# Kernel tuning notes

Hardware: AMD Instinct MI355X
Metric: run time of the kernel (lower is better)

The kernel has to match this reference:

```python
import jax, jax.numpy as jnp
import numpy as np

C, L, M, DEPTH = 32, 4, 128, 7
DIM = (L ** (DEPTH + 1) - 1) // (L - 1)  # 21845 nodes, complete 4-ary tree, BFS order


def _level_starts(dim, fanout):
    # start offset of each BFS level of a complete `fanout`-ary tree
    starts = [0]
    n = 1
    while starts[-1] + n < dim:
        starts.append(starts[-1] + n)
        n *= fanout
    starts.append(dim)
    return starts  # level d occupies [starts[d], starts[d+1])


def setup_inputs() -> dict:
    key = jax.random.key(0)
    ks = jax.random.split(key, 5)
    return {
        "labels": jax.random.randint(ks[0], (DIM,), 0, M, dtype=jnp.int32),
        "A": jax.random.normal(ks[1], (C, C, L), jnp.float32),
        "B": jax.random.normal(ks[2], (C, M), jnp.float32),
        "Pi": jax.random.normal(ks[3], (C, L), jnp.float32),
        "SP": jax.random.normal(ks[4], (L,), jnp.float32),
    }


def _htmm_log_likelihood(labels, A, B, Pi, SP):
    dim = labels.shape[0]
    c, m = B.shape
    fan = A.shape[2]
    starts = _level_starts(dim, fan)
    D = len(starts) - 2  # deepest level index (leaves)

    # softmax reparameterization (dims as in torch source)
    smA = jax.nn.softmax(A, axis=0)   # (C,C,L)
    smB = jax.nn.softmax(B, axis=1)   # (C,M)
    smPi = jax.nn.softmax(Pi, axis=0)  # (C,L)
    smSP = jax.nn.softmax(SP, axis=0)  # (L,)

    n_leaves = starts[D + 1] - starts[D]
    leaf_pos = jnp.arange(n_leaves) % fan          # child position of each leaf
    leaf_labels = labels[starts[D]:]

    # ---- upward pass ----
    beta_leaf = smPi[:, leaf_pos].T * smB[:, leaf_labels].T  # (n_leaves,C)
    beta_leaf = beta_leaf / beta_leaf.sum(1, keepdims=True)
    beta = jnp.zeros((dim, c), A.dtype).at[starts[D]:].set(beta_leaf)
    t_beta = jnp.zeros((dim, c), A.dtype)
    A_SP = smA * smSP[None, None, :]  # (C,C,L): SP[pos] * A[:,:,pos]

    for d in range(D - 1, -1, -1):
        n_p = starts[d + 1] - starts[d]
        beta_ch = beta[starts[d + 1]:starts[d + 2]].reshape(n_p, fan, c)  # (P,L,C)
        # t_beta_u[i] = sum_l SP[l] * sum_j A[i,j,l] * beta_child_l[j]
        tb = jnp.einsum('ijl,plj->pi', A_SP, beta_ch)  # (P,C)
        bl = tb * smB[:, labels[starts[d]:starts[d + 1]]].T
        bl = bl / bl.sum(1, keepdims=True)
        t_beta = t_beta.at[starts[d]:starts[d + 1]].set(tb)
        beta = beta.at[starts[d]:starts[d + 1]].set(bl)

    # ---- downward pass ----
    eps = jnp.zeros((dim, c), A.dtype).at[0].set(beta[0])
    t_eps = jnp.zeros((dim, c, c, fan), A.dtype)
    for d in range(D):
        n_p = starts[d + 1] - starts[d]
        beta_ch = beta[starts[d + 1]:starts[d + 2]].reshape(n_p, fan, c)  # (P,L,C)
        eps_pa = eps[starts[d]:starts[d + 1]]    # (P,C)
        tb_pa = t_beta[starts[d]:starts[d + 1]]  # (P,C)
        # t_eps_u[j,i,l] = beta[ch_l,i] * SP[l]*A[j,i,l] * eps_u[j] / t_beta_u[j]
        te = (beta_ch.transpose(0, 2, 1)[:, None, :, :]   # (P,1,C_i,L)
              * A_SP[None]                                  # (1,C_j,C_i,L)
              * (eps_pa / tb_pa)[:, :, None, None])         # (P,C_j,1,1)
        t_eps = t_eps.at[starts[d]:starts[d + 1]].set(te)
        eps_ch = te.sum(1).transpose(0, 2, 1).reshape(-1, c)  # sum_j -> (P,L,C) -> (P*L,C)
        eps = eps.at[starts[d + 1]:starts[d + 2]].set(eps_ch)

    # ---- log-likelihood ----
    ll = (t_eps * jnp.log(smA)[None]).sum()
    ll = ll + (eps * jnp.log(smB)[:, labels].T).sum()
    ll = ll + (eps[starts[D]:] * jnp.log(smPi)[:, leaf_pos].T).sum()
    ll = ll + (t_eps * jnp.log(smSP)[None, None, None, :]).sum()
    return ll


def reference(labels, A, B, Pi, SP):
    return _htmm_log_likelihood(labels, A, B, Pi, SP)
```

## Files before the change

kernel.cpp:

```cpp
#include <hip/hip_runtime.h>


static constexpr int OFF_B4   = 0;
static constexpr int OFF_PART = 8192;
static constexpr int IC2      = 9760;
static constexpr int IROOT2   = 10272;

__device__ __forceinline__ float rsum32(float v) {
#pragma unroll
  for (int k = 1; k <= 16; k <<= 1) v += __shfl_xor(v, k);
  return v;
}
__device__ __forceinline__ void rsum32x2(float& a, float& b) {
#pragma unroll
  for (int k = 1; k <= 16; k <<= 1) { a += __shfl_xor(a, k); b += __shfl_xor(b, k); }
}
__device__ __forceinline__ void rsum32x4(float& a, float& b, float& c, float& d) {
#pragma unroll
  for (int k = 1; k <= 16; k <<= 1) {
    a += __shfl_xor(a, k); b += __shfl_xor(b, k);
    c += __shfl_xor(c, k); d += __shfl_xor(d, k);
  }
}
__device__ __forceinline__ float4 exp4f(float4 v) {
  return make_float4(__expf(v.x), __expf(v.y), __expf(v.z), __expf(v.w));
}

#define W_DECL float4 Wr0, Wr1, Wr2, Wr3, Wr4, Wr5, Wr6, Wr7, Wr8, Wr9,     \
    Wr10, Wr11, Wr12, Wr13, Wr14, Wr15, Wr16, Wr17, Wr18, Wr19, Wr20, Wr21, \
    Wr22, Wr23, Wr24, Wr25, Wr26, Wr27, Wr28, Wr29, Wr30, Wr31;

#define REPW(X) X(0,Wr0) X(1,Wr1) X(2,Wr2) X(3,Wr3) X(4,Wr4) X(5,Wr5)       \
    X(6,Wr6) X(7,Wr7) X(8,Wr8) X(9,Wr9) X(10,Wr10) X(11,Wr11) X(12,Wr12)    \
    X(13,Wr13) X(14,Wr14) X(15,Wr15) X(16,Wr16) X(17,Wr17) X(18,Wr18)       \
    X(19,Wr19) X(20,Wr20) X(21,Wr21) X(22,Wr22) X(23,Wr23) X(24,Wr24)       \
    X(25,Wr25) X(26,Wr26) X(27,Wr27) X(28,Wr28) X(29,Wr29) X(30,Wr30)       \
    X(31,Wr31)

#define REPQ(X) X(0,Wr0,Wr1,Wr2,Wr3) X(1,Wr4,Wr5,Wr6,Wr7)                   \
    X(2,Wr8,Wr9,Wr10,Wr11) X(3,Wr12,Wr13,Wr14,Wr15) X(4,Wr16,Wr17,Wr18,Wr19)\
    X(5,Wr20,Wr21,Wr22,Wr23) X(6,Wr24,Wr25,Wr26,Wr27) X(7,Wr28,Wr29,Wr30,Wr31)

#define WLD_B(J, WJ) WJ = *(const float4*)(scrW_ + 4 * (J));
#define W_LOADUP { const float* scrW_ = scr + lane * 132; REPW(WLD_B) }

#define DOT_B(J, WJ) { const float4 x_ = *(const float4*)(dXp_ + 4 * (J));   \
    dt0_ = fmaf(WJ.x, x_.x, dt0_); dt1_ = fmaf(WJ.y, x_.y, dt1_);            \
    dt2_ = fmaf(WJ.z, x_.z, dt2_); dt3_ = fmaf(WJ.w, x_.w, dt3_); }
#define DOT128M(OUT, XP) { const float* dXp_ = (XP);                         \
    float dt0_ = 0.f, dt1_ = 0.f, dt2_ = 0.f, dt3_ = 0.f;                    \
    REPW(DOT_B) (OUT) = (dt0_ + dt1_) + (dt2_ + dt3_); }

#define DOTX2_B(J, WJ) {                                                     \
    const float4 x_ = *(const float4*)(dXp0_ + 4 * (J));                     \
    const float4 y_ = *(const float4*)(dXp1_ + 4 * (J));                     \
    da0_ = fmaf(WJ.x, x_.x, da0_); db0_ = fmaf(WJ.x, y_.x, db0_);            \
    da1_ = fmaf(WJ.y, x_.y, da1_); db1_ = fmaf(WJ.y, y_.y, db1_);            \
    da2_ = fmaf(WJ.z, x_.z, da2_); db2_ = fmaf(WJ.z, y_.z, db2_);            \
    da3_ = fmaf(WJ.w, x_.w, da3_); db3_ = fmaf(WJ.w, y_.w, db3_); }
#define DOT128X2M(O0, O1, XP0, XP1) {                                        \
    const float* dXp0_ = (XP0); const float* dXp1_ = (XP1);                  \
    float da0_ = 0.f, da1_ = 0.f, da2_ = 0.f, da3_ = 0.f;                    \
    float db0_ = 0.f, db1_ = 0.f, db2_ = 0.f, db3_ = 0.f;                    \
    REPW(DOTX2_B) (O0) = (da0_ + da1_) + (da2_ + da3_);                      \
    (O1) = (db0_ + db1_) + (db2_ + db3_); }

#define WO_B(Q, WA, WB, WC, WD) {                                            \
    const float4 rv_ = *(const float4*)(rbp_ + 4 * (Q));                     \
    ww0_ = fmaf(WA.x, rv_.x, ww0_); ww1_ = fmaf(WA.y, rv_.x, ww1_);          \
    ww2_ = fmaf(WA.z, rv_.x, ww2_); ww3_ = fmaf(WA.w, rv_.x, ww3_);          \
    ww0_ = fmaf(WB.x, rv_.y, ww0_); ww1_ = fmaf(WB.y, rv_.y, ww1_);          \
    ww2_ = fmaf(WB.z, rv_.y, ww2_); ww3_ = fmaf(WB.w, rv_.y, ww3_);          \
    ww0_ = fmaf(WC.x, rv_.z, ww0_); ww1_ = fmaf(WC.y, rv_.z, ww1_);          \
    ww2_ = fmaf(WC.z, rv_.z, ww2_); ww3_ = fmaf(WC.w, rv_.z, ww3_);          \
    ww0_ = fmaf(WD.x, rv_.w, ww0_); ww1_ = fmaf(WD.y, rv_.w, ww1_);          \
    ww2_ = fmaf(WD.z, rv_.w, ww2_); ww3_ = fmaf(WD.w, rv_.w, ww3_); }
#define WONLY128M(W, RBP) { const float* rbp_ = (RBP);                       \
    float ww0_ = 0.f, ww1_ = 0.f, ww2_ = 0.f, ww3_ = 0.f;                    \
    REPQ(WO_B) (W)[0] = ww0_; (W)[1] = ww1_; (W)[2] = ww2_; (W)[3] = ww3_; }

#define WU_SUB(ROW, WX, RC) {                                                \
    const float4 av_ = *(const float4*)(ALGp_ + (ROW) * 128);                \
    ww0_ = fmaf(WX.x, RC, ww0_); uu0_ = fmaf(av_.x, RC, uu0_);               \
    ww1_ = fmaf(WX.y, RC, ww1_); uu1_ = fmaf(av_.y, RC, uu1_);               \
    ww2_ = fmaf(WX.z, RC, ww2_); uu2_ = fmaf(av_.z, RC, uu2_);               \
    ww3_ = fmaf(WX.w, RC, ww3_); uu3_ = fmaf(av_.w, RC, uu3_); }
#define WU_B(Q, WA, WB, WC, WD) {                                            \
    const float4 rv_ = *(const float4*)(rbp_ + 4 * (Q));                     \
    WU_SUB(4 * (Q) + 0, WA, rv_.x) WU_SUB(4 * (Q) + 1, WB, rv_.y)            \
    WU_SUB(4 * (Q) + 2, WC, rv_.z) WU_SUB(4 * (Q) + 3, WD, rv_.w) }
#define WU128M(W, U, RBP) { const float* rbp_ = (RBP);                       \
    const float* ALGp_ = scr + lane * 4;                                     \
    float ww0_ = 0.f, ww1_ = 0.f, ww2_ = 0.f, ww3_ = 0.f;                    \
    float uu0_ = 0.f, uu1_ = 0.f, uu2_ = 0.f, uu3_ = 0.f;                    \
    REPQ(WU_B) (W)[0] = ww0_; (W)[1] = ww1_; (W)[2] = ww2_; (W)[3] = ww3_;   \
    (U)[0] = uu0_; (U)[1] = uu1_; (U)[2] = uu2_; (U)[3] = uu3_; }

#define WUX2_SUB(ROW, WX, RC0, RC1) {                                        \
    const float4 av_ = *(const float4*)(ALGp_ + (ROW) * 128);                \
    wa0_ = fmaf(WX.x, RC0, wa0_); wb0_ = fmaf(WX.x, RC1, wb0_);              \
    ua0_ = fmaf(av_.x, RC0, ua0_); ub0_ = fmaf(av_.x, RC1, ub0_);            \
    wa1_ = fmaf(WX.y, RC0, wa1_); wb1_ = fmaf(WX.y, RC1, wb1_);              \
    ua1_ = fmaf(av_.y, RC0, ua1_); ub1_ = fmaf(av_.y, RC1, ub1_);            \
    wa2_ = fmaf(WX.z, RC0, wa2_); wb2_ = fmaf(WX.z, RC1, wb2_);              \
    ua2_ = fmaf(av_.z, RC0, ua2_); ub2_ = fmaf(av_.z, RC1, ub2_);            \
    wa3_ = fmaf(WX.w, RC0, wa3_); wb3_ = fmaf(WX.w, RC1, wb3_);              \
    ua3_ = fmaf(av_.w, RC0, ua3_); ub3_ = fmaf(av_.w, RC1, ub3_); }
#define WUX2_B(Q, WA, WB, WC, WD) {                                          \
    const float4 rv0_ = *(const float4*)(rbp0_ + 4 * (Q));                   \
    const float4 rv1_ = *(const float4*)(rbp1_ + 4 * (Q));                   \
    WUX2_SUB(4 * (Q) + 0, WA, rv0_.x, rv1_.x)                                \
    WUX2_SUB(4 * (Q) + 1, WB, rv0_.y, rv1_.y)                                \
    WUX2_SUB(4 * (Q) + 2, WC, rv0_.z, rv1_.z)                                \
    WUX2_SUB(4 * (Q) + 3, WD, rv0_.w, rv1_.w) }
#define WU128X2M(W0, U0, W1, U1, RBP0, RBP1) {                               \
    const float* rbp0_ = (RBP0); const float* rbp1_ = (RBP1);                \
    const float* ALGp_ = scr + lane * 4;                                     \
    float wa0_ = 0.f, wa1_ = 0.f, wa2_ = 0.f, wa3_ = 0.f;                    \
    float ua0_ = 0.f, ua1_ = 0.f, ua2_ = 0.f, ua3_ = 0.f;                    \
    float wb0_ = 0.f, wb1_ = 0.f, wb2_ = 0.f, wb3_ = 0.f;                    \
    float ub0_ = 0.f, ub1_ = 0.f, ub2_ = 0.f, ub3_ = 0.f;                    \
    REPQ(WUX2_B)                                                             \
    (W0)[0] = wa0_; (W0)[1] = wa1_; (W0)[2] = wa2_; (W0)[3] = wa3_;          \
    (U0)[0] = ua0_; (U0)[1] = ua1_; (U0)[2] = ua2_; (U0)[3] = ua3_;          \
    (W1)[0] = wb0_; (W1)[1] = wb1_; (W1)[2] = wb2_; (W1)[3] = wb3_;          \
    (U1)[0] = ub0_; (U1)[1] = ub1_; (U1)[2] = ub2_; (U1)[3] = ub3_; }

#define WRD_B(J, WJ) { const float4 av = A4[(J) * 32 + lane];                \
    const float4 e = exp4f(av);                                              \
    const float4 asp = make_float4(e.x * inv4.x, e.y * inv4.y,               \
                                   e.z * inv4.z, e.w * inv4.w);              \
    WJ = asp;                                                                \
    if (grp == ((J) >> 1))                                                   \
      *(float4*)(scr + (J) * 128 + lane * 4) =                               \
          make_float4(asp.x * (av.x - sub4.x), asp.y * (av.y - sub4.y),      \
                      asp.z * (av.z - sub4.z), asp.w * (av.w - sub4.w)); }

__global__ __launch_bounds__(256, 1) void k_up(const int* __restrict__ labels,
                                               const float* __restrict__ A,
                                               const float* __restrict__ B,
                                               const float* __restrict__ Pi,
                                               const float* __restrict__ SP,
                                               float* __restrict__ ws) {
  __shared__ __align__(16) float scr[4224];
  __shared__ __align__(16) float regB[4224];
  __shared__ __align__(16) float sPt[132];
  __shared__ int labs[425];
  const int t = threadIdx.x, lane = t & 31, grp = t >> 5;
  const int s = blockIdx.x;
  int* wsi = (int*)ws;
  const float4* A4 = (const float4*)A;
  const float4* B4 = (const float4*)B;

  if (t < 16) wsi[IC2 + 32 * t] = 0;
  else if (t == 16) wsi[IROOT2] = 0;

  const float sv0 = SP[0], sv1 = SP[1], sv2 = SP[2], sv3 = SP[3];
  const float sp0 = __expf(sv0), sp1 = __expf(sv1), sp2 = __expf(sv2), sp3 = __expf(sv3);
  const float spsum = sp0 + sp1 + sp2 + sp3;
  const float spinv = 1.f / spsum;
  float4 c4 = make_float4(0.f, 0.f, 0.f, 0.f);
  for (int i = 0; i < 32; ++i) {
    const float4 e = exp4f(A4[i * 32 + lane]);
    c4.x += e.x; c4.y += e.y; c4.z += e.z; c4.w += e.w;
  }
  const float4 inv4 = make_float4(sp0 * spinv / c4.x, sp1 * spinv / c4.y,
                                  sp2 * spinv / c4.z, sp3 * spinv / c4.w);
#pragma unroll
  for (int k = 0; k < 4; ++k) {
    const int i = grp * 4 + k;
    const float4 e = exp4f(A4[i * 32 + lane]);
    *(float4*)(scr + i * 132 + 4 * lane) =
        make_float4(e.x * inv4.x, e.y * inv4.y, e.z * inv4.z, e.w * inv4.w);
  }
#pragma unroll
  for (int rI = 0; rI < 4; ++rI) {
    const int i = grp + rI * 8;
    const float4 e = exp4f(B4[i * 32 + lane]);
    const float sinv = 1.f / rsum32(e.x + e.y + e.z + e.w);
    regB[(4 * lane + 0) * 33 + i] = e.x * sinv;
    regB[(4 * lane + 1) * 33 + i] = e.y * sinv;
    regB[(4 * lane + 2) * 33 + i] = e.z * sinv;
    regB[(4 * lane + 3) * 33 + i] = e.w * sinv;
  }
  if (grp < 4) {
    const float e = __expf(Pi[lane * 4 + grp]);
    sPt[grp * 33 + lane] = e / rsum32(e);
  }
  if (t < 84) {
    int g, d;
    if (t < 4) { g = 341 + 4 * s + t; d = 341 + t; }
    else if (t < 20) { g = 1365 + 16 * s + (t - 4); d = 345 + (t - 4); }
    else { g = 5461 + 64 * s + (t - 20); d = 361 + (t - 20); }
    labs[d] = labels[g];
  }
  if (t == 84) labs[85 + (s & 255)] = labels[85 + s];
  __syncthreads();
  W_DECL
  W_LOADUP
  __syncthreads();

#pragma unroll
  for (int h = 0; h < 2; ++h) {
    const int q0 = grp + 32 * h, q1 = q0 + 8, q2 = q0 + 16, q3 = q0 + 24;
    float v0 = sPt[(q0 & 3) * 33 + lane] * regB[labs[361 + q0] * 33 + lane];
    float v1 = sPt[(q1 & 3) * 33 + lane] * regB[labs[361 + q1] * 33 + lane];
    float v2 = sPt[(q2 & 3) * 33 + lane] * regB[labs[361 + q2] * 33 + lane];
    float v3 = sPt[(q3 & 3) * 33 + lane] * regB[labs[361 + q3] * 33 + lane];
    float s0 = v0, s1 = v1, s2 = v2, s3 = v3;
    rsum32x4(s0, s1, s2, s3);
    scr[(q0 >> 2) * 128 + lane * 4 + (q0 & 3)] = v0 / s0;
    scr[(q1 >> 2) * 128 + lane * 4 + (q1 & 3)] = v1 / s1;
    scr[(q2 >> 2) * 128 + lane * 4 + (q2 & 3)] = v2 / s2;
    scr[(q3 >> 2) * 128 + lane * 4 + (q3 & 3)] = v3 / s3;
  }
  __syncthreads();
  {
    const int p0 = grp, p1 = grp + 8;
    float tb0, tb1;
    DOT128X2M(tb0, tb1, scr + p0 * 128, scr + p1 * 128)
    float bl0 = tb0 * regB[labs[345 + p0] * 33 + lane];
    float bl1 = tb1 * regB[labs[345 + p1] * 33 + lane];
    float s0 = bl0, s1 = bl1;
    rsum32x2(s0, s1);
    bl0 /= s0; bl1 /= s1;
    scr[2048 + (p0 >> 2) * 128 + lane * 4 + (p0 & 3)] = bl0;
    scr[2048 + (p1 >> 2) * 128 + lane * 4 + (p1 & 3)] = bl1;
  }
  __syncthreads();
  if (grp < 4) {
    float tb;
    DOT128M(tb, scr + 2048 + grp * 128)
    float bl = tb * regB[labs[341 + grp] * 33 + lane];
    bl /= rsum32(bl);
    scr[2560 + lane * 4 + grp] = bl;
  }
  __syncthreads();
  if (grp == 0) {
    float tb;
    DOT128M(tb, scr + 2560)
    float bl = tb * regB[labs[85 + (s & 255)] * 33 + lane];
    bl /= rsum32(bl);
    ws[OFF_B4 + s * 32 + lane] = bl;
  }
}

__global__ __launch_bounds__(512, 1)
void k_down(const int* __restrict__ labels,
            const float* __restrict__ A,
            const float* __restrict__ B,
            const float* __restrict__ Pi,
            const float* __restrict__ SP,
            float* __restrict__ ws,
            float* __restrict__ out) {
  __shared__ __align__(16) float scr[6144];
  __shared__ __align__(16) float regB[4224];
  __shared__ __align__(16) float sPt[132];
  __shared__ __align__(16) float tbrT[2720];
  __shared__ __align__(16) float tbS[672];
  __shared__ __align__(16) float ownb[32];
  __shared__ __align__(16) float r_buf[512];
  __shared__ int labs[425];
  __shared__ int fin;
  const int t = threadIdx.x, lane = t & 31, grp = t >> 5;
  const int s = blockIdx.x;
  int* wsi = (int*)ws;
  double* partd = (double*)(ws + OFF_PART);
  const float4* A4 = (const float4*)A;
  const float4* B4 = (const float4*)B;

  float pf0[8], pf1[8];
#pragma unroll
  for (int h = 0; h < 2; ++h) {
    const int p0 = grp + 32 * h, p1 = p0 + 16;
#pragma unroll
    for (int l = 0; l < 4; ++l) {
      pf0[h * 4 + l] = ws[OFF_B4 + (p0 * 4 + l) * 32 + lane];
      pf1[h * 4 + l] = ws[OFF_B4 + (p1 * 4 + l) * 32 + lane];
    }
  }

  const float sv0 = SP[0], sv1 = SP[1], sv2 = SP[2], sv3 = SP[3];
  const float sp0 = __expf(sv0), sp1 = __expf(sv1), sp2 = __expf(sv2), sp3 = __expf(sv3);
  const float spsum = sp0 + sp1 + sp2 + sp3;
  const float spinv = 1.f / spsum;
  const float lss = __logf(spsum);
  float4 c4 = make_float4(0.f, 0.f, 0.f, 0.f);
  for (int i = 0; i < 32; ++i) {
    const float4 e = exp4f(A4[i * 32 + lane]);
    c4.x += e.x; c4.y += e.y; c4.z += e.z; c4.w += e.w;
  }
  const float4 inv4 = make_float4(sp0 * spinv / c4.x, sp1 * spinv / c4.y,
                                  sp2 * spinv / c4.z, sp3 * spinv / c4.w);
  const float4 sub4 = make_float4(__logf(c4.x) - (sv0 - lss), __logf(c4.y) - (sv1 - lss),
                                  __logf(c4.z) - (sv2 - lss), __logf(c4.w) - (sv3 - lss));
#pragma unroll
  for (int k = 0; k < 2; ++k) {
    const int i = grp * 2 + k;
    const float4 e = exp4f(A4[i * 32 + lane]);
    *(float4*)(scr + i * 132 + 4 * lane) =
        make_float4(e.x * inv4.x, e.y * inv4.y, e.z * inv4.z, e.w * inv4.w);
  }
#pragma unroll
  for (int rI = 0; rI < 2; ++rI) {
    const int i = grp + rI * 16;
    const float4 e = exp4f(B4[i * 32 + lane]);
    const float sinv = 1.f / rsum32(e.x + e.y + e.z + e.w);
    regB[(4 * lane + 0) * 33 + i] = e.x * sinv;
    regB[(4 * lane + 1) * 33 + i] = e.y * sinv;
    regB[(4 * lane + 2) * 33 + i] = e.z * sinv;
    regB[(4 * lane + 3) * 33 + i] = e.w * sinv;
  }
  if (grp < 4) {
    const float e = __expf(Pi[lane * 4 + grp]);
    sPt[grp * 33 + lane] = e / rsum32(e);
  }
  for (int idx = t; idx < 341; idx += 512) labs[idx] = labels[idx];
  if (t < 84) {
    int g, d;
    if (t < 4) { g = 341 + 4 * s + t; d = 341 + t; }
    else if (t < 20) { g = 1365 + 16 * s + (t - 4); d = 345 + (t - 4); }
    else { g = 5461 + 64 * s + (t - 20); d = 361 + (t - 20); }
    labs[d] = labels[g];
  }
  __syncthreads();
  W_DECL
  W_LOADUP
  __syncthreads();

  {
    const int q0 = grp, q1 = grp + 16, q2 = grp + 32, q3 = grp + 48;
    float v0 = sPt[(q0 & 3) * 33 + lane] * regB[labs[361 + q0] * 33 + lane];
    float v1 = sPt[(q1 & 3) * 33 + lane] * regB[labs[361 + q1] * 33 + lane];
    float v2 = sPt[(q2 & 3) * 33 + lane] * regB[labs[361 + q2] * 33 + lane];
    float v3 = sPt[(q3 & 3) * 33 + lane] * regB[labs[361 + q3] * 33 + lane];
    float s0 = v0, s1 = v1, s2 = v2, s3 = v3;
    rsum32x4(s0, s1, s2, s3);
    scr[(q0 >> 2) * 128 + lane * 4 + (q0 & 3)] = v0 / s0;
    scr[(q1 >> 2) * 128 + lane * 4 + (q1 & 3)] = v1 / s1;
    scr[(q2 >> 2) * 128 + lane * 4 + (q2 & 3)] = v2 / s2;
    scr[(q3 >> 2) * 128 + lane * 4 + (q3 & 3)] = v3 / s3;
  }
  __syncthreads();
  if (grp < 8) {
    const int p0 = grp, p1 = grp + 8;
    float tb0, tb1;
    DOT128X2M(tb0, tb1, scr + p0 * 128, scr + p1 * 128)
    float bl0 = tb0 * regB[labs[345 + p0] * 33 + lane];
    float bl1 = tb1 * regB[labs[345 + p1] * 33 + lane];
    float s0 = bl0, s1 = bl1;
    rsum32x2(s0, s1);
    bl0 /= s0; bl1 /= s1;
    tbS[(5 + p0) * 32 + lane] = tb0;
    tbS[(5 + p1) * 32 + lane] = tb1;
    scr[2048 + (p0 >> 2) * 128 + lane * 4 + (p0 & 3)] = bl0;
    scr[2048 + (p1 >> 2) * 128 + lane * 4 + (p1 & 3)] = bl1;
  }
  __syncthreads();
  if (grp < 4) {
    float tb;
    DOT128M(tb, scr + 2048 + grp * 128)
    float bl = tb * regB[labs[341 + grp] * 33 + lane];
    bl /= rsum32(bl);
    tbS[(1 + grp) * 32 + lane] = tb;
    scr[2560 + lane * 4 + grp] = bl;
  }
  __syncthreads();
  if (grp == 0) {
    float tb;
    DOT128M(tb, scr + 2560)
    float bl = tb * regB[labs[85 + s] * 33 + lane];
    bl /= rsum32(bl);
    tbS[lane] = tb;
    ownb[lane] = bl;
  }
  __syncthreads();

#pragma unroll
  for (int h = 0; h < 2; ++h) {
    const int p0 = grp + 32 * h, p1 = p0 + 16;
    float* st0 = scr + grp * 128;
    float* st1 = scr + 2048 + grp * 128;
#pragma unroll
    for (int l = 0; l < 4; ++l) {
      st0[lane * 4 + l] = pf0[h * 4 + l];
      st1[lane * 4 + l] = pf1[h * 4 + l];
    }
    float tb0, tb1;
    DOT128X2M(tb0, tb1, st0, st1)
    float bl0 = tb0 * regB[labs[21 + p0] * 33 + lane];
    float bl1 = tb1 * regB[labs[21 + p1] * 33 + lane];
    float s0 = bl0, s1 = bl1;
    rsum32x2(s0, s1);
    bl0 /= s0; bl1 /= s1;
    tbrT[(21 + p0) * 32 + lane] = tb0;
    tbrT[(21 + p1) * 32 + lane] = tb1;
    scr[4096 + (p0 >> 2) * 128 + lane * 4 + (p0 & 3)] = bl0;
    scr[4096 + (p1 >> 2) * 128 + lane * 4 + (p1 & 3)] = bl1;
  }
  __syncthreads();
  {
    const int p = grp;
    float tb;
    DOT128M(tb, scr + 4096 + p * 128)
    float bl = tb * regB[labs[5 + p] * 33 + lane];
    bl /= rsum32(bl);
    tbrT[(5 + p) * 32 + lane] = tb;
    scr[(p >> 2) * 128 + lane * 4 + (p & 3)] = bl;
  }
  __syncthreads();
  if (grp < 4) {
    float tb;
    DOT128M(tb, scr + grp * 128)
    float bl = tb * regB[labs[1 + grp] * 33 + lane];
    bl /= rsum32(bl);
    tbrT[(1 + grp) * 32 + lane] = tb;
    scr[512 + lane * 4 + grp] = bl;
  }
  __syncthreads();
  if (grp == 0) { float tb; DOT128M(tb, scr + 512) tbrT[lane] = tb; }
  __syncthreads();

  for (int idx = t; idx < 4224; idx += 512) regB[idx] = __logf(regB[idx]);
  if (t < 132) sPt[t] = __logf(sPt[t]);
  REPW(WRD_B)
  __syncthreads();

  double ll = 0.0;
  float eps4own = 0.f;
  if (grp < 4) {
    const int n1 = 1 + (s >> 6), n2 = 5 + (s >> 4), n3 = 21 + (s >> 2);
    const int a0 = s >> 6, a1 = (s >> 4) & 3, a2 = (s >> 2) & 3, a3 = s & 3;
    float w[4], uv[4];
    float* rb = r_buf + grp * 32;

    float tbv = tbrT[lane];
    float bcv = tbv * __expf(regB[labs[0] * 33 + lane]);
    bcv /= rsum32(bcv);
    rb[lane] = bcv / tbv;
    if (grp == 0 && s == 0) {
      ll += (double)(bcv * regB[labs[0] * 33 + lane]);
      WU128M(w, uv, rb)
      const float lb0 = regB[labs[1] * 33 + lane], lb1 = regB[labs[2] * 33 + lane];
      const float lb2 = regB[labs[3] * 33 + lane], lb3 = regB[labs[4] * 33 + lane];
      float b0 = tbrT[1 * 32 + lane] * __expf(lb0);
      float b1 = tbrT[2 * 32 + lane] * __expf(lb1);
      float b2 = tbrT[3 * 32 + lane] * __expf(lb2);
      float b3 = tbrT[4 * 32 + lane] * __expf(lb3);
      float s0 = b0, s1 = b1, s2 = b2, s3 = b3;
      rsum32x4(s0, s1, s2, s3);
      b0 /= s0; b1 /= s1; b2 /= s2; b3 /= s3;
      ll += (double)(b0 * uv[0]) + (double)(b0 * w[0] * lb0);
      ll += (double)(b1 * uv[1]) + (double)(b1 * w[1] * lb1);
      ll += (double)(b2 * uv[2]) + (double)(b2 * w[2] * lb2);
      ll += (double)(b3 * uv[3]) + (double)(b3 * w[3] * lb3);
    } else {
      WONLY128M(w, rb)
    }

    tbv = tbrT[n1 * 32 + lane];
    bcv = tbv * __expf(regB[labs[n1] * 33 + lane]);
    bcv /= rsum32(bcv);
    rb[lane] = (bcv * w[a0]) / tbv;
    if (grp == 1 && (s & 63) == 0) {
      WU128M(w, uv, rb)
      const int cb = 5 + 4 * (s >> 6);
      const float lb0 = regB[labs[cb + 0] * 33 + lane], lb1 = regB[labs[cb + 1] * 33 + lane];
      const float lb2 = regB[labs[cb + 2] * 33 + lane], lb3 = regB[labs[cb + 3] * 33 + lane];
      float b0 = tbrT[(cb + 0) * 32 + lane] * __expf(lb0);
      float b1 = tbrT[(cb + 1) * 32 + lane] * __expf(lb1);
      float b2 = tbrT[(cb + 2) * 32 + lane] * __expf(lb2);
      float b3 = tbrT[(cb + 3) * 32 + lane] * __expf(lb3);
      float s0 = b0, s1 = b1, s2 = b2, s3 = b3;
      rsum32x4(s0, s1, s2, s3);
      b0 /= s0; b1 /= s1; b2 /= s2; b3 /= s3;
      ll += (double)(b0 * uv[0]) + (double)(b0 * w[0] * lb0);
      ll += (double)(b1 * uv[1]) + (double)(b1 * w[1] * lb1);
      ll += (double)(b2 * uv[2]) + (double)(b2 * w[2] * lb2);
      ll += (double)(b3 * uv[3]) + (double)(b3 * w[3] * lb3);
    } else {
      WONLY128M(w, rb)
    }

    tbv = tbrT[n2 * 32 + lane];
    bcv = tbv * __expf(regB[labs[n2] * 33 + lane]);
    bcv /= rsum32(bcv);
    rb[lane] = (bcv * w[a1]) / tbv;
    if (grp == 2 && (s & 15) == 0) {
      WU128M(w, uv, rb)
      const int cb = 21 + 4 * (s >> 4);
      const float lb0 = regB[labs[cb + 0] * 33 + lane], lb1 = regB[labs[cb + 1] * 33 + lane];
      const float lb2 = regB[labs[cb + 2] * 33 + lane], lb3 = regB[labs[cb + 3] * 33 + lane];
      float b0 = tbrT[(cb + 0) * 32 + lane] * __expf(lb0);
      float b1 = tbrT[(cb + 1) * 32 + lane] * __expf(lb1);
      float b2 = tbrT[(cb + 2) * 32 + lane] * __expf(lb2);
      float b3 = tbrT[(cb + 3) * 32 + lane] * __expf(lb3);
      float s0 = b0, s1 = b1, s2 = b2, s3 = b3;
      rsum32x4(s0, s1, s2, s3);
      b0 /= s0; b1 /= s1; b2 /= s2; b3 /= s3;
      ll += (double)(b0 * uv[0]) + (double)(b0 * w[0] * lb0);
      ll += (double)(b1 * uv[1]) + (double)(b1 * w[1] * lb1);
      ll += (double)(b2 * uv[2]) + (double)(b2 * w[2] * lb2);
      ll += (double)(b3 * uv[3]) + (double)(b3 * w[3] * lb3);
    } else {
      WONLY128M(w, rb)
    }

    tbv = tbrT[n3 * 32 + lane];
    bcv = tbv * __expf(regB[labs[n3] * 33 + lane]);
    bcv /= rsum32(bcv);
    rb[lane] = (bcv * w[a2]) / tbv;
    if (grp == 3 && (s & 3) == 0) {
      WU128M(w, uv, rb)
      const int cb = s & ~3;
#pragma unroll
      for (int l = 0; l < 4; ++l) {
        const int ci = cb + l;
        const float bc = ws[OFF_B4 + ci * 32 + lane];
        const float e = bc * w[l];
        ll += (double)(bc * uv[l]) + (double)(e * regB[labs[85 + ci] * 33 + lane]);
      }
    } else {
      WONLY128M(w, rb)
    }
    eps4own = ownb[lane] * w[a3];
  }
  __syncthreads();

  if (grp == 0) {
    r_buf[lane] = eps4own / tbS[lane];
    float w[4], u[4];
    WU128M(w, u, r_buf)
#pragma unroll
    for (int l = 0; l < 4; ++l) {
      const int lab = labs[341 + l];
      const float tbv = tbS[(1 + l) * 32 + lane];
      float bcv = tbv * __expf(regB[lab * 33 + lane]);
      bcv /= rsum32(bcv);
      const float e = bcv * w[l];
      ll += (double)(bcv * u[l]) + (double)(e * regB[lab * 33 + lane]);
      tbS[(1 + l) * 32 + lane] = e / tbv;
    }
  }
  __syncthreads();
  if (grp < 4) {
    const int p = grp;
    r_buf[p * 32 + lane] = tbS[(1 + p) * 32 + lane];
    float w[4], u[4];
    WU128M(w, u, r_buf + p * 32)
#pragma unroll
    for (int l = 0; l < 4; ++l) {
      const int q = p * 4 + l;
      const int lab = labs[345 + q];
      const float tbv = tbS[(5 + q) * 32 + lane];
      float bcv = tbv * __expf(regB[lab * 33 + lane]);
      bcv /= rsum32(bcv);
      const float e = bcv * w[l];
      ll += (double)(bcv * u[l]) + (double)(e * regB[lab * 33 + lane]);
      tbS[(5 + q) * 32 + lane] = e / tbv;
    }
  }
  __syncthreads();
  if (grp < 8) {
    const int p0 = grp, p1 = grp + 8;
    float* rb0 = r_buf + grp * 32;
    float* rb1 = r_buf + 256 + grp * 32;
    rb0[lane] = tbS[(5 + p0) * 32 + lane];
    rb1[lane] = tbS[(5 + p1) * 32 + lane];
    float w0[4], u0[4], w1[4], u1[4];
    WU128X2M(w0, u0, w1, u1, rb0, rb1)
#pragma unroll
    for (int l = 0; l < 4; ++l) {
      const int q0 = p0 * 4 + l, q1 = p1 * 4 + l;
      const float lb0 = regB[labs[361 + q0] * 33 + lane];
      const float lb1 = regB[labs[361 + q1] * 33 + lane];
      const float lp = sPt[l * 33 + lane];
      float b0 = __expf(lp + lb0);
      float b1 = __expf(lp + lb1);
      float s0 = b0, s1 = b1;
      rsum32x2(s0, s1);
      b0 /= s0; b1 /= s1;
      const float e0 = b0 * w0[l], e1 = b1 * w1[l];
      ll += (double)(b0 * u0[l]) + (double)(e0 * lb0) + (double)(e0 * lp);
      ll += (double)(b1 * u1[l]) + (double)(e1 * lb1) + (double)(e1 * lp);
    }
  }

#pragma unroll
  for (int k = 32; k >= 1; k >>= 1) ll += __shfl_xor(ll, k);
  double* rbd = (double*)r_buf;
  __syncthreads();
  if ((t & 63) == 0) rbd[t >> 6] = ll;
  __syncthreads();
  if (t == 0) {
    partd[s] = ((rbd[0] + rbd[1]) + (rbd[2] + rbd[3])) +
               ((rbd[4] + rbd[5]) + (rbd[6] + rbd[7]));
    __threadfence();
    int f = 0;
    if (atomicAdd(&wsi[IC2 + 32 * (s >> 4)], 1) == 15)
      if (atomicAdd(&wsi[IROOT2], 1) == 15) f = 1;
    fin = f;
  }
  __syncthreads();
  if (fin) {
    __threadfence();
    if (t < 64) {
      double v = 0.0;
      for (int k = t; k < 256; k += 64) v += partd[k];
#pragma unroll
      for (int k = 32; k >= 1; k >>= 1) v += __shfl_xor(v, k);
      if (t == 0) out[0] = (float)v;
    }
  }
}

extern "C" void kernel_launch(void* const* d_in, const int* in_sizes, int n_in,
                              void* d_out, int out_size, void* d_ws, size_t ws_size,
                              hipStream_t stream) {
  (void)in_sizes; (void)n_in; (void)out_size; (void)ws_size;
  const int* labels = (const int*)d_in[0];
  const float* A = (const float*)d_in[1];
  const float* B = (const float*)d_in[2];
  const float* Pi = (const float*)d_in[3];
  const float* SP = (const float*)d_in[4];
  float* ws = (float*)d_ws;
  float* out = (float*)d_out;

  hipLaunchKernelGGL(k_up, dim3(256), dim3(256), 0, stream,
                     labels, A, B, Pi, SP, ws);
  hipLaunchKernelGGL(k_down, dim3(256), dim3(512), 0, stream,
                     labels, A, B, Pi, SP, ws, out);
}
```

Baseline: 106.4 us.

## Precompute softmax tables and subtree t_beta in up pass, reuse in down pass

The up kernel now runs with 512 threads. Block 0 writes the normalized A_SP, the softmaxed B, log B, log Pi and the A*logA tables to workspace. Every block also stores its subtree's t_beta values. The down kernel loads these instead of recomputing the softmaxes and the bottom upward levels, which removes redundant exp/log work and one set of dot products per block. In exchange it adds workspace traffic and depends on a workspace-size check; when the workspace is too small it falls back to the old kernels.

```diff
diff --git a/kernel.cpp b/kernel.cpp
--- a/kernel.cpp
+++ b/kernel.cpp
@@ -5,6 +5,13 @@
 static constexpr int OFF_PART = 8192;
 static constexpr int IC2      = 9760;
 static constexpr int IROOT2   = 10272;
+static constexpr int OFF_ASP  = 10304;
+static constexpr int OFF_RB   = 14528;
+static constexpr int OFF_LRB  = 18752;
+static constexpr int OFF_LSP  = 22976;
+static constexpr int OFF_ALG  = 23120;
+static constexpr int OFF_TBO  = 27216;
+static constexpr size_t WS_NEED_BYTES = (size_t)(OFF_TBO + 256 * 672) * 4;
 
 __device__ __forceinline__ float rsum32(float v) {
 #pragma unroll
@@ -43,6 +50,8 @@
 
 #define WLD_B(J, WJ) WJ = *(const float4*)(scrW_ + 4 * (J));
 #define W_LOADUP { const float* scrW_ = scr + lane * 132; REPW(WLD_B) }
+
+#define WLDDN_B(J, WJ) WJ = *(const float4*)(wsASP_ + (J) * 132 + lane * 4);
 
 #define DOT_B(J, WJ) { const float4 x_ = *(const float4*)(dXp_ + 4 * (J));   \
     dt0_ = fmaf(WJ.x, x_.x, dt0_); dt1_ = fmaf(WJ.y, x_.y, dt1_);            \
@@ -136,12 +145,12 @@
           make_float4(asp.x * (av.x - sub4.x), asp.y * (av.y - sub4.y),      \
                       asp.z * (av.z - sub4.z), asp.w * (av.w - sub4.w)); }
 
-__global__ __launch_bounds__(256, 1) void k_up(const int* __restrict__ labels,
-                                               const float* __restrict__ A,
-                                               const float* __restrict__ B,
-                                               const float* __restrict__ Pi,
-                                               const float* __restrict__ SP,
-                                               float* __restrict__ ws) {
+__global__ __launch_bounds__(256, 1) void k_up_f(const int* __restrict__ labels,
+                                                 const float* __restrict__ A,
+                                                 const float* __restrict__ B,
+                                                 const float* __restrict__ Pi,
+                                                 const float* __restrict__ SP,
+                                                 float* __restrict__ ws) {
   __shared__ __align__(16) float scr[4224];
   __shared__ __align__(16) float regB[4224];
   __shared__ __align__(16) float sPt[132];
@@ -246,13 +255,13 @@
 }
 
 __global__ __launch_bounds__(512, 1)
-void k_down(const int* __restrict__ labels,
-            const float* __restrict__ A,
-            const float* __restrict__ B,
-            const float* __restrict__ Pi,
-            const float* __restrict__ SP,
-            float* __restrict__ ws,
-            float* __restrict__ out) {
+void k_down_f(const int* __restrict__ labels,
+              const float* __restrict__ A,
+              const float* __restrict__ B,
+              const float* __restrict__ Pi,
+              const float* __restrict__ SP,
+              float* __restrict__ ws,
+              float* __restrict__ out) {
   __shared__ __align__(16) float scr[6144];
   __shared__ __align__(16) float regB[4224];
   __shared__ __align__(16) float sPt[132];
@@ -614,10 +623,439 @@
   }
 }
 
+__global__ __launch_bounds__(512, 1) void k_up_p(const int* __restrict__ labels,
+                                                 const float* __restrict__ A,
+                                                 const float* __restrict__ B,
+                                                 const float* __restrict__ Pi,
+                                                 const float* __restrict__ SP,
+                                                 float* __restrict__ ws) {
+  __shared__ __align__(16) float scr[4224];
+  __shared__ __align__(16) float regB[4224];
+  __shared__ __align__(16) float sPt[132];
+  __shared__ int labs[425];
+  const int t = threadIdx.x, lane = t & 31, grp = t >> 5;
+  const int s = blockIdx.x;
+  int* wsi = (int*)ws;
+  const float4* A4 = (const float4*)A;
+  const float4* B4 = (const float4*)B;
+
+  if (t < 16) wsi[IC2 + 32 * t] = 0;
+  else if (t == 16) wsi[IROOT2] = 0;
+
+  const float sv0 = SP[0], sv1 = SP[1], sv2 = SP[2], sv3 = SP[3];
+  const float sp0 = __expf(sv0), sp1 = __expf(sv1), sp2 = __expf(sv2), sp3 = __expf(sv3);
+  const float spsum = sp0 + sp1 + sp2 + sp3;
+  const float spinv = 1.f / spsum;
+  const float lss = __logf(spsum);
+  float4 c4 = make_float4(0.f, 0.f, 0.f, 0.f);
+  for (int i = 0; i < 32; ++i) {
+    const float4 e = exp4f(A4[i * 32 + lane]);
+    c4.x += e.x; c4.y += e.y; c4.z += e.z; c4.w += e.w;
+  }
+  const float4 inv4 = make_float4(sp0 * spinv / c4.x, sp1 * spinv / c4.y,
+                                  sp2 * spinv / c4.z, sp3 * spinv / c4.w);
+  const float4 sub4 = make_float4(__logf(c4.x) - (sv0 - lss), __logf(c4.y) - (sv1 - lss),
+                                  __logf(c4.z) - (sv2 - lss), __logf(c4.w) - (sv3 - lss));
+#pragma unroll
+  for (int k = 0; k < 2; ++k) {
+    const int i = grp * 2 + k;
+    const float4 e = exp4f(A4[i * 32 + lane]);
+    *(float4*)(scr + i * 132 + 4 * lane) =
+        make_float4(e.x * inv4.x, e.y * inv4.y, e.z * inv4.z, e.w * inv4.w);
+  }
+#pragma unroll
+  for (int rI = 0; rI < 2; ++rI) {
+    const int i = grp + rI * 16;
+    const float4 e = exp4f(B4[i * 32 + lane]);
+    const float sinv = 1.f / rsum32(e.x + e.y + e.z + e.w);
+    regB[(4 * lane + 0) * 33 + i] = e.x * sinv;
+    regB[(4 * lane + 1) * 33 + i] = e.y * sinv;
+    regB[(4 * lane + 2) * 33 + i] = e.z * sinv;
+    regB[(4 * lane + 3) * 33 + i] = e.w * sinv;
+  }
+  if (grp < 4) {
+    const float e = __expf(Pi[lane * 4 + grp]);
+    sPt[grp * 33 + lane] = e / rsum32(e);
+  } else if (grp == 4) {
+    if (lane < 4) sPt[lane * 33 + 32] = 1.f;
+  }
+  if (t < 84) {
+    int g, d;
+    if (t < 4) { g = 341 + 4 * s + t; d = 341 + t; }
+    else if (t < 20) { g = 1365 + 16 * s + (t - 4); d = 345 + (t - 4); }
+    else { g = 5461 + 64 * s + (t - 20); d = 361 + (t - 20); }
+    labs[d] = labels[g];
+  }
+  if (t == 84) labs[85 + (s & 255)] = labels[85 + s];
+  __syncthreads();
+
+  if (s == 0) {
+    for (int idx = t; idx < 4224; idx += 512) {
+      ws[OFF_ASP + idx] = scr[idx];
+      const float v = regB[idx];
+      ws[OFF_RB + idx] = v;
+      ws[OFF_LRB + idx] = __logf(v);
+    }
+    if (t < 132) ws[OFF_LSP + t] = __logf(sPt[t]);
+#pragma unroll
+    for (int k = 0; k < 2; ++k) {
+      const int i = grp * 2 + k;
+      const float4 av = A4[i * 32 + lane];
+      const float4 e = exp4f(av);
+      const float4 asp = make_float4(e.x * inv4.x, e.y * inv4.y,
+                                     e.z * inv4.z, e.w * inv4.w);
+      *(float4*)(ws + OFF_ALG + i * 128 + lane * 4) =
+          make_float4(asp.x * (av.x - sub4.x), asp.y * (av.y - sub4.y),
+                      asp.z * (av.z - sub4.z), asp.w * (av.w - sub4.w));
+    }
+  }
+  W_DECL
+  W_LOADUP
+  __syncthreads();
+
+  float* tbs = ws + OFF_TBO + s * 672;
+  {
+    const int q0 = grp, q1 = grp + 16, q2 = grp + 32, q3 = grp + 48;
+    float v0 = sPt[(q0 & 3) * 33 + lane] * regB[labs[361 + q0] * 33 + lane];
+    float v1 = sPt[(q1 & 3) * 33 + lane] * regB[labs[361 + q1] * 33 + lane];
+    float v2 = sPt[(q2 & 3) * 33 + lane] * regB[labs[361 + q2] * 33 + lane];
+    float v3 = sPt[(q3 & 3) * 33 + lane] * regB[labs[361 + q3] * 33 + lane];
+    float s0 = v0, s1 = v1, s2 = v2, s3 = v3;
+    rsum32x4(s0, s1, s2, s3);
+    scr[(q0 >> 2) * 128 + lane * 4 + (q0 & 3)] = v0 / s0;
+    scr[(q1 >> 2) * 128 + lane * 4 + (q1 & 3)] = v1 / s1;
+    scr[(q2 >> 2) * 128 + lane * 4 + (q2 & 3)] = v2 / s2;
+    scr[(q3 >> 2) * 128 + lane * 4 + (q3 & 3)] = v3 / s3;
+  }
+  __syncthreads();
+  if (grp < 8) {
+    const int p0 = grp, p1 = grp + 8;
+    float tb0, tb1;
+    DOT128X2M(tb0, tb1, scr + p0 * 128, scr + p1 * 128)
+    float bl0 = tb0 * regB[labs[345 + p0] * 33 + lane];
+    float bl1 = tb1 * regB[labs[345 + p1] * 33 + lane];
+    float s0 = bl0, s1 = bl1;
+    rsum32x2(s0, s1);
+    bl0 /= s0; bl1 /= s1;
+    tbs[(5 + p0) * 32 + lane] = tb0;
+    tbs[(5 + p1) * 32 + lane] = tb1;
+    scr[2048 + (p0 >> 2) * 128 + lane * 4 + (p0 & 3)] = bl0;
+    scr[2048 + (p1 >> 2) * 128 + lane * 4 + (p1 & 3)] = bl1;
+  }
+  __syncthreads();
+  if (grp < 4) {
+    float tb;
+    DOT128M(tb, scr + 2048 + grp * 128)
+    float bl = tb * regB[labs[341 + grp] * 33 + lane];
+    bl /= rsum32(bl);
+    tbs[(1 + grp) * 32 + lane] = tb;
+    scr[2560 + lane * 4 + grp] = bl;
+  }
+  __syncthreads();
+  if (grp == 0) {
+    float tb;
+    DOT128M(tb, scr + 2560)
+    float bl = tb * regB[labs[85 + (s & 255)] * 33 + lane];
+    bl /= rsum32(bl);
+    tbs[lane] = tb;
+    ws[OFF_B4 + s * 32 + lane] = bl;
+  }
+}
+
+__global__ __launch_bounds__(512, 1)
+void k_down_p(const int* __restrict__ labels,
+              const float* __restrict__ ws_c,
+              float* __restrict__ ws,
+              float* __restrict__ out) {
+  __shared__ __align__(16) float scr[6144];
+  __shared__ __align__(16) float regB[4224];
+  __shared__ __align__(16) float sPt[132];
+  __shared__ __align__(16) float tbrT[2720];
+  __shared__ __align__(16) float tbS[672];
+  __shared__ __align__(16) float ownb[32];
+  __shared__ __align__(16) float r_buf[512];
+  __shared__ int labs[425];
+  __shared__ int fin;
+  const int t = threadIdx.x, lane = t & 31, grp = t >> 5;
+  const int s = blockIdx.x;
+  int* wsi = (int*)ws;
+  double* partd = (double*)(ws + OFF_PART);
+  (void)ws_c;
+
+  float pf0[8], pf1[8];
+#pragma unroll
+  for (int h = 0; h < 2; ++h) {
+    const int p0 = grp + 32 * h, p1 = p0 + 16;
+#pragma unroll
+    for (int l = 0; l < 4; ++l) {
+      pf0[h * 4 + l] = ws[OFF_B4 + (p0 * 4 + l) * 32 + lane];
+      pf1[h * 4 + l] = ws[OFF_B4 + (p1 * 4 + l) * 32 + lane];
+    }
+  }
+
+  for (int idx = t; idx < 4224; idx += 512) scr[idx] = ws[OFF_ASP + idx];
+  for (int idx = t; idx < 4224; idx += 512) regB[idx] = ws[OFF_RB + idx];
+  if (t < 132) sPt[t] = ws[OFF_LSP + t];
+  for (int idx = t; idx < 672; idx += 512) tbS[idx] = ws[OFF_TBO + s * 672 + idx];
+  if (t < 32) ownb[t] = ws[OFF_B4 + s * 32 + t];
+  for (int idx = t; idx < 341; idx += 512) labs[idx] = labels[idx];
+  if (t < 84) {
+    int g, d;
+    if (t < 4) { g = 341 + 4 * s + t; d = 341 + t; }
+    else if (t < 20) { g = 1365 + 16 * s + (t - 4); d = 345 + (t - 4); }
+    else { g = 5461 + 64 * s + (t - 20); d = 361 + (t - 20); }
+    labs[d] = labels[g];
+  }
+  __syncthreads();
+  W_DECL
+  W_LOADUP
+  __syncthreads();
+
+#pragma unroll
+  for (int h = 0; h < 2; ++h) {
+    const int p0 = grp + 32 * h, p1 = p0 + 16;
+    float* st0 = scr + grp * 128;
+    float* st1 = scr + 2048 + grp * 128;
+#pragma unroll
+    for (int l = 0; l < 4; ++l) {
+      st0[lane * 4 + l] = pf0[h * 4 + l];
+      st1[lane * 4 + l] = pf1[h * 4 + l];
+    }
+    float tb0, tb1;
+    DOT128X2M(tb0, tb1, st0, st1)
+    float bl0 = tb0 * regB[labs[21 + p0] * 33 + lane];
+    float bl1 = tb1 * regB[labs[21 + p1] * 33 + lane];
+    float s0 = bl0, s1 = bl1;
+    rsum32x2(s0, s1);
+    bl0 /= s0; bl1 /= s1;
+    tbrT[(21 + p0) * 32 + lane] = tb0;
+    tbrT[(21 + p1) * 32 + lane] = tb1;
+    scr[4096 + (p0 >> 2) * 128 + lane * 4 + (p0 & 3)] = bl0;
+    scr[4096 + (p1 >> 2) * 128 + lane * 4 + (p1 & 3)] = bl1;
+  }
+  __syncthreads();
+  {
+    const int p = grp;
+    float tb;
+    DOT128M(tb, scr + 4096 + p * 128)
+    float bl = tb * regB[labs[5 + p] * 33 + lane];
+    bl /= rsum32(bl);
+    tbrT[(5 + p) * 32 + lane] = tb;
+    scr[(p >> 2) * 128 + lane * 4 + (p & 3)] = bl;
+  }
+  __syncthreads();
+  if (grp < 4) {
+    float tb;
+    DOT128M(tb, scr + grp * 128)
+    float bl = tb * regB[labs[1 + grp] * 33 + lane];
+    bl /= rsum32(bl);
+    tbrT[(1 + grp) * 32 + lane] = tb;
+    scr[512 + lane * 4 + grp] = bl;
+  }
+  __syncthreads();
+  if (grp == 0) { float tb; DOT128M(tb, scr + 512) tbrT[lane] = tb; }
+  __syncthreads();
+
+  for (int idx = t; idx < 4096; idx += 512) scr[idx] = ws[OFF_ALG + idx];
+  for (int idx = t; idx < 4224; idx += 512) regB[idx] = ws[OFF_LRB + idx];
+  if (grp < 8) {
+    const float* wsASP_ = ws + OFF_ASP;
+    REPW(WLDDN_B)
+  }
+  __syncthreads();
+
+  double ll = 0.0;
+  float eps4own = 0.f;
+  if (grp < 4) {
+    const int n1 = 1 + (s >> 6), n2 = 5 + (s >> 4), n3 = 21 + (s >> 2);
+    const int a0 = s >> 6, a1 = (s >> 4) & 3, a2 = (s >> 2) & 3, a3 = s & 3;
+    float w[4], uv[4];
+    float* rb = r_buf + grp * 32;
+
+    float tbv = tbrT[lane];
+    float bcv = tbv * __expf(regB[labs[0] * 33 + lane]);
+    bcv /= rsum32(bcv);
+    rb[lane] = bcv / tbv;
+    if (grp == 0 && s == 0) {
+      ll += (double)(bcv * regB[labs[0] * 33 + lane]);
+      WU128M(w, uv, rb)
+      const float lb0 = regB[labs[1] * 33 + lane], lb1 = regB[labs[2] * 33 + lane];
+      const float lb2 = regB[labs[3] * 33 + lane], lb3 = regB[labs[4] * 33 + lane];
+      float b0 = tbrT[1 * 32 + lane] * __expf(lb0);
+      float b1 = tbrT[2 * 32 + lane] * __expf(lb1);
+      float b2 = tbrT[3 * 32 + lane] * __expf(lb2);
+      float b3 = tbrT[4 * 32 + lane] * __expf(lb3);
+      float s0 = b0, s1 = b1, s2 = b2, s3 = b3;
+      rsum32x4(s0, s1, s2, s3);
+      b0 /= s0; b1 /= s1; b2 /= s2; b3 /= s3;
+      ll += (double)(b0 * uv[0]) + (double)(b0 * w[0] * lb0);
+      ll += (double)(b1 * uv[1]) + (double)(b1 * w[1] * lb1);
+      ll += (double)(b2 * uv[2]) + (double)(b2 * w[2] * lb2);
+      ll += (double)(b3 * uv[3]) + (double)(b3 * w[3] * lb3);
+    } else {
+      WONLY128M(w, rb)
+    }
+
+    tbv = tbrT[n1 * 32 + lane];
+    bcv = tbv * __expf(regB[labs[n1] * 33 + lane]);
+    bcv /= rsum32(bcv);
+    rb[lane] = (bcv * w[a0]) / tbv;
+    if (grp == 1 && (s & 63) == 0) {
+      WU128M(w, uv, rb)
+      const int cb = 5 + 4 * (s >> 6);
+      const float lb0 = regB[labs[cb + 0] * 33 + lane], lb1 = regB[labs[cb + 1] * 33 + lane];
+      const float lb2 = regB[labs[cb + 2] * 33 + lane], lb3 = regB[labs[cb + 3] * 33 + lane];
+      float b0 = tbrT[(cb + 0) * 32 + lane] * __expf(lb0);
+      float b1 = tbrT[(cb + 1) * 32 + lane] * __expf(lb1);
+      float b2 = tbrT[(cb + 2) * 32 + lane] * __expf(lb2);
+      float b3 = tbrT[(cb + 3) * 32 + lane] * __expf(lb3);
+      float s0 = b0, s1 = b1, s2 = b2, s3 = b3;
+      rsum32x4(s0, s1, s2, s3);
+      b0 /= s0; b1 /= s1; b2 /= s2; b3 /= s3;
+      ll += (double)(b0 * uv[0]) + (double)(b0 * w[0] * lb0);
+      ll += (double)(b1 * uv[1]) + (double)(b1 * w[1] * lb1);
+      ll += (double)(b2 * uv[2]) + (double)(b2 * w[2] * lb2);
+      ll += (double)(b3 * uv[3]) + (double)(b3 * w[3] * lb3);
+    } else {
+      WONLY128M(w, rb)
+    }
+
+    tbv = tbrT[n2 * 32 + lane];
+    bcv = tbv * __expf(regB[labs[n2] * 33 + lane]);
+    bcv /= rsum32(bcv);
+    rb[lane] = (bcv * w[a1]) / tbv;
+    if (grp == 2 && (s & 15) == 0) {
+      WU128M(w, uv, rb)
+      const int cb = 21 + 4 * (s >> 4);
+      const float lb0 = regB[labs[cb + 0] * 33 + lane], lb1 = regB[labs[cb + 1] * 33 + lane];
+      const float lb2 = regB[labs[cb + 2] * 33 + lane], lb3 = regB[labs[cb + 3] * 33 + lane];
+      float b0 = tbrT[(cb + 0) * 32 + lane] * __expf(lb0);
+      float b1 = tbrT[(cb + 1) * 32 + lane] * __expf(lb1);
+      float b2 = tbrT[(cb + 2) * 32 + lane] * __expf(lb2);
+      float b3 = tbrT[(cb + 3) * 32 + lane] * __expf(lb3);
+      float s0 = b0, s1 = b1, s2 = b2, s3 = b3;
+      rsum32x4(s0, s1, s2, s3);
+      b0 /= s0; b1 /= s1; b2 /= s2; b3 /= s3;
+      ll += (double)(b0 * uv[0]) + (double)(b0 * w[0] * lb0);
+      ll += (double)(b1 * uv[1]) + (double)(b1 * w[1] * lb1);
+      ll += (double)(b2 * uv[2]) + (double)(b2 * w[2] * lb2);
+      ll += (double)(b3 * uv[3]) + (double)(b3 * w[3] * lb3);
+    } else {
+      WONLY128M(w, rb)
+    }
+
+    tbv = tbrT[n3 * 32 + lane];
+    bcv = tbv * __expf(regB[labs[n3] * 33 + lane]);
+    bcv /= rsum32(bcv);
+    rb[lane] = (bcv * w[a2]) / tbv;
+    if (grp == 3 && (s & 3) == 0) {
+      WU128M(w, uv, rb)
+      const int cb = s & ~3;
+#pragma unroll
+      for (int l = 0; l < 4; ++l) {
+        const int ci = cb + l;
+        const float bc = ws[OFF_B4 + ci * 32 + lane];
+        const float e = bc * w[l];
+        ll += (double)(bc * uv[l]) + (double)(e * regB[labs[85 + ci] * 33 + lane]);
+      }
+    } else {
+      WONLY128M(w, rb)
+    }
+    eps4own = ownb[lane] * w[a3];
+  }
+  __syncthreads();
+
+  if (grp == 0) {
+    r_buf[lane] = eps4own / tbS[lane];
+    float w[4], u[4];
+    WU128M(w, u, r_buf)
+#pragma unroll
+    for (int l = 0; l < 4; ++l) {
+      const int lab = labs[341 + l];
+      const float tbv = tbS[(1 + l) * 32 + lane];
+      float bcv = tbv * __expf(regB[lab * 33 + lane]);
+      bcv /= rsum32(bcv);
+      const float e = bcv * w[l];
+      ll += (double)(bcv * u[l]) + (double)(e * regB[lab * 33 + lane]);
+      tbS[(1 + l) * 32 + lane] = e / tbv;
+    }
+  }
+  __syncthreads();
+  if (grp < 4) {
+    const int p = grp;
+    r_buf[p * 32 + lane] = tbS[(1 + p) * 32 + lane];
+    float w[4], u[4];
+    WU128M(w, u, r_buf + p * 32)
+#pragma unroll
+    for (int l = 0; l < 4; ++l) {
+      const int q = p * 4 + l;
+      const int lab = labs[345 + q];
+      const float tbv = tbS[(5 + q) * 32 + lane];
+      float bcv = tbv * __expf(regB[lab * 33 + lane]);
+      bcv /= rsum32(bcv);
+      const float e = bcv * w[l];
+      ll += (double)(bcv * u[l]) + (double)(e * regB[lab * 33 + lane]);
+      tbS[(5 + q) * 32 + lane] = e / tbv;
+    }
+  }
+  __syncthreads();
+  if (grp < 8) {
+    const int p0 = grp, p1 = grp + 8;
+    float* rb0 = r_buf + grp * 32;
+    float* rb1 = r_buf + 256 + grp * 32;
+    rb0[lane] = tbS[(5 + p0) * 32 + lane];
+    rb1[lane] = tbS[(5 + p1) * 32 + lane];
+    float w0[4], u0[4], w1[4], u1[4];
+    WU128X2M(w0, u0, w1, u1, rb0, rb1)
+#pragma unroll
+    for (int l = 0; l < 4; ++l) {
+      const int q0 = p0 * 4 + l, q1 = p1 * 4 + l;
+      const float lb0 = regB[labs[361 + q0] * 33 + lane];
+      const float lb1 = regB[labs[361 + q1] * 33 + lane];
+      const float lp = sPt[l * 33 + lane];
+      float b0 = __expf(lp + lb0);
+      float b1 = __expf(lp + lb1);
+      float s0 = b0, s1 = b1;
+      rsum32x2(s0, s1);
+      b0 /= s0; b1 /= s1;
+      const float e0 = b0 * w0[l], e1 = b1 * w1[l];
+      ll += (double)(b0 * u0[l]) + (double)(e0 * lb0) + (double)(e0 * lp);
+      ll += (double)(b1 * u1[l]) + (double)(e1 * lb1) + (double)(e1 * lp);
+    }
+  }
+
+#pragma unroll
+  for (int k = 32; k >= 1; k >>= 1) ll += __shfl_xor(ll, k);
+  double* rbd = (double*)r_buf;
+  __syncthreads();
+  if ((t & 63) == 0) rbd[t >> 6] = ll;
+  __syncthreads();
+  if (t == 0) {
+    partd[s] = ((rbd[0] + rbd[1]) + (rbd[2] + rbd[3])) +
+               ((rbd[4] + rbd[5]) + (rbd[6] + rbd[7]));
+    __threadfence();
+    int f = 0;
+    if (atomicAdd(&wsi[IC2 + 32 * (s >> 4)], 1) == 15)
+      if (atomicAdd(&wsi[IROOT2], 1) == 15) f = 1;
+    fin = f;
+  }
+  __syncthreads();
+  if (fin) {
+    __threadfence();
+    if (t < 64) {
+      double v = 0.0;
+      for (int k = t; k < 256; k += 64) v += partd[k];
+#pragma unroll
+      for (int k = 32; k >= 1; k >>= 1) v += __shfl_xor(v, k);
+      if (t == 0) out[0] = (float)v;
+    }
+  }
+}
+
 extern "C" void kernel_launch(void* const* d_in, const int* in_sizes, int n_in,
                               void* d_out, int out_size, void* d_ws, size_t ws_size,
                               hipStream_t stream) {
-  (void)in_sizes; (void)n_in; (void)out_size; (void)ws_size;
+  (void)in_sizes; (void)n_in; (void)out_size;
   const int* labels = (const int*)d_in[0];
   const float* A = (const float*)d_in[1];
   const float* B = (const float*)d_in[2];
@@ -626,8 +1064,15 @@
   float* ws = (float*)d_ws;
   float* out = (float*)d_out;
 
-  hipLaunchKernelGGL(k_up, dim3(256), dim3(256), 0, stream,
-                     labels, A, B, Pi, SP, ws);
-  hipLaunchKernelGGL(k_down, dim3(256), dim3(512), 0, stream,
-                     labels, A, B, Pi, SP, ws, out);
+  if (ws_size >= WS_NEED_BYTES) {
+    hipLaunchKernelGGL(k_up_p, dim3(256), dim3(512), 0, stream,
+                       labels, A, B, Pi, SP, ws);
+    hipLaunchKernelGGL(k_down_p, dim3(256), dim3(512), 0, stream,
+                       labels, ws, ws, out);
+  } else {
+    hipLaunchKernelGGL(k_up_f, dim3(256), dim3(256), 0, stream,
+                       labels, A, B, Pi, SP, ws);
+    hipLaunchKernelGGL(k_down_f, dim3(256), dim3(512), 0, stream,
+                       labels, A, B, Pi, SP, ws, out);
+  }
 }
```

Result: no change. 105.6 us (-0.8%).
